# Performance work log

Measured on AMD Instinct MI355X. Metric: run time of the kernel, lower is better.

The kernel has to match this reference:

```python
import jax, jax.numpy as jnp
import numpy as np

N = 100000   # nodes
D = 128      # feature dim
E = 1600000  # edges (avg degree 16)
BN_EPS = 1e-5


def setup_inputs() -> dict:
    key = jax.random.key(0)
    ks = jax.random.split(key, 8)
    x = jax.random.normal(ks[0], (N, D), dtype=jnp.float32)
    edge_index = jax.random.randint(ks[1], (2, E), 0, N, dtype=jnp.int64)
    W = jax.random.normal(ks[2], (D, D), dtype=jnp.float32) * 0.05   # GCNConv linear weight
    b = jax.random.normal(ks[3], (D,), dtype=jnp.float32) * 0.05     # GCNConv bias
    gamma = jax.random.uniform(ks[4], (D,), dtype=jnp.float32) + 0.5 # BN weight
    beta = jax.random.normal(ks[5], (D,), dtype=jnp.float32) * 0.1   # BN bias
    running_mean = jax.random.normal(ks[6], (D,), dtype=jnp.float32) * 0.1
    running_var = jax.random.uniform(ks[7], (D,), dtype=jnp.float32) + 0.5
    return {"x": x, "edge_index": edge_index, "W": W, "b": b,
            "gamma": gamma, "beta": beta,
            "running_mean": running_mean, "running_var": running_var}


def reference(x, edge_index, W, b, gamma, beta, running_mean, running_var):
    # --- GCNConv (default: add self-loops, symmetric normalization) ---
    h = x @ W                                        # [N, D]
    loops = jnp.arange(N, dtype=edge_index.dtype)
    src = jnp.concatenate([edge_index[0], loops])    # [E+N]
    dst = jnp.concatenate([edge_index[1], loops])    # [E+N]
    deg = jax.ops.segment_sum(jnp.ones_like(dst, dtype=h.dtype), dst, num_segments=N)
    dinv = jax.lax.rsqrt(jnp.maximum(deg, 1.0))      # deg >= 1 due to self-loops
    norm = dinv[src] * dinv[dst]                     # [E+N]
    agg = jax.ops.segment_sum(h[src] * norm[:, None], dst, num_segments=N)  # [N, D]
    agg = agg + b
    # --- BatchNorm1d (inference: running stats) ---
    bn = (agg - running_mean) * jax.lax.rsqrt(running_var + BN_EPS) * gamma + beta
    # --- ReLU + residual (dropout is identity in eval) ---
    return jax.nn.relu(bn) + x
```

## Files before the change

kernel.cpp:

```cpp
#include <hip/hip_runtime.h>

#define D 128
#define BN_EPS 1e-5f
#define NBUCK 512
#define BSHIFT 8
#define BNODES 256

using short8 = __attribute__((ext_vector_type(8))) short;
using floatx4 = __attribute__((ext_vector_type(4))) float;

__device__ inline unsigned short f2bf(float f) {
    unsigned u = __float_as_uint(f);
    u += 0x7fff + ((u >> 16) & 1);
    return (unsigned short)(u >> 16);
}
__device__ inline float bf2f(unsigned short s) {
    return __uint_as_float(((unsigned)s) << 16);
}

__global__ void wt_kernel(const float* __restrict__ W, const float* __restrict__ b,
                          const float* __restrict__ gamma, const float* __restrict__ beta,
                          const float* __restrict__ mean, const float* __restrict__ var,
                          unsigned short* __restrict__ Wt, float* __restrict__ scv,
                          float* __restrict__ pov) {
    int t = blockIdx.x * blockDim.x + threadIdx.x;
    int k = t >> 7, n = t & 127;
    Wt[(size_t)n * D + k] = f2bf(W[t]);
    if (t < D) {
        float sc = gamma[t] * rsqrtf(var[t] + BN_EPS);
        scv[t] = sc;
        pov[t] = (b[t] - mean[t]) * sc + beta[t];
    }
}

__global__ __launch_bounds__(512) void pAwt_kernel(
    const int* __restrict__ dst, int* __restrict__ bucketTot, int E,
    const float* __restrict__ W, const float* __restrict__ b,
    const float* __restrict__ gamma, const float* __restrict__ beta,
    const float* __restrict__ mean, const float* __restrict__ var,
    unsigned short* __restrict__ Wt, float* __restrict__ scv,
    float* __restrict__ pov) {
    __shared__ int lh[NBUCK];
    int tid = threadIdx.x;
    lh[tid] = 0;
    __syncthreads();
    for (int i = blockIdx.x * 512 + tid; i < E; i += gridDim.x * 512)
        atomicAdd(&lh[dst[i] >> BSHIFT], 1);
    if (blockIdx.x < 16) {
        int t = blockIdx.x * 512 + tid;
#pragma unroll
        for (int h = 0; h < 2; ++h) {
            int tt = t + h * 8192;
            Wt[(size_t)(tt & 127) * D + (tt >> 7)] = f2bf(W[tt]);
        }
        if (blockIdx.x == 0 && tid < D) {
            float sc = gamma[tid] * rsqrtf(var[tid] + BN_EPS);
            scv[tid] = sc;
            pov[tid] = (b[tid] - mean[tid]) * sc + beta[tid];
        }
    }
    __syncthreads();
    if (lh[tid]) atomicAdd(&bucketTot[tid], lh[tid]);
}

__global__ __launch_bounds__(512) void pB_kernel(const int* __restrict__ src,
                                                 const int* __restrict__ dst,
                                                 const int* __restrict__ bucketTot,
                                                 int* __restrict__ resCnt,
                                                 int2* __restrict__ pairs, int E) {
    __shared__ int sb[NBUCK];
    __shared__ int lh[NBUCK];
    __shared__ int lcur[NBUCK];
    int tid = threadIdx.x;
    sb[tid] = bucketTot[tid];
    lh[tid] = 0;
    __syncthreads();
    for (int d = 1; d < NBUCK; d <<= 1) {
        int v = (tid >= d) ? sb[tid - d] : 0;
        __syncthreads();
        sb[tid] += v;
        __syncthreads();
    }
    int chunk = (E + gridDim.x - 1) / gridDim.x;
    int base = blockIdx.x * chunk;
    int lim = min(chunk, E - base);
    if (lim <= 0) return;
    for (int i = tid; i < lim; i += 512) atomicAdd(&lh[dst[base + i] >> BSHIFT], 1);
    __syncthreads();
    int c = lh[tid];
    lcur[tid] = c ? (sb[tid] - bucketTot[tid]) + atomicAdd(&resCnt[tid], c) : 0;
    __syncthreads();
    for (int i = tid; i < lim; i += 512) {
        int s = src[base + i], d2 = dst[base + i];
        int pos = atomicAdd(&lcur[d2 >> BSHIFT], 1);
        pairs[pos] = make_int2(s, d2);
    }
}

__global__ __launch_bounds__(512) void sortxs_kernel(
    const int2* __restrict__ pairs, const int* __restrict__ bucketTot,
    const float* __restrict__ x, int* __restrict__ deg, int* __restrict__ offs,
    int* __restrict__ colidx, float* __restrict__ dinv,
    unsigned short* __restrict__ xs, int N, int E) {
    __shared__ int sb[NBUCK];
    __shared__ int lh[BNODES];
    __shared__ int lcur[BNODES];
    __shared__ float sdv[BNODES];
    int tid = threadIdx.x;
    int b = blockIdx.x;
    sb[tid] = bucketTot[tid];
    __syncthreads();
    for (int d = 1; d < NBUCK; d <<= 1) {
        int v = (tid >= d) ? sb[tid - d] : 0;
        __syncthreads();
        sb[tid] += v;
        __syncthreads();
    }
    int cnt = bucketTot[b];
    int base = sb[b] - cnt;
    if (tid < BNODES) lh[tid] = 0;
    __syncthreads();
    for (int i = tid; i < cnt; i += 512)
        atomicAdd(&lh[pairs[base + i].y & (BNODES - 1)], 1);
    __syncthreads();
    int orig = (tid < BNODES) ? lh[tid] : 0;
    for (int d = 1; d < BNODES; d <<= 1) {
        int v = (tid < BNODES && tid >= d) ? lh[tid - d] : 0;
        __syncthreads();
        if (tid < BNODES) lh[tid] += v;
        __syncthreads();
    }
    if (tid < BNODES) {
        int exc = lh[tid] - orig;
        int node = b * BNODES + tid;
        float dvv = rsqrtf((float)(orig + 1));
        sdv[tid] = dvv;
        if (node < N) {
            deg[node] = orig;
            offs[node] = base + exc;
            dinv[node] = dvv;
        }
        lcur[tid] = exc;
    }
    if (b == 0 && tid == 0) offs[N] = E;
    __syncthreads();
    for (int i = tid; i < cnt; i += 512) {
        int2 p = pairs[base + i];
        int pos = atomicAdd(&lcur[p.y & (BNODES - 1)], 1);
        colidx[base + pos] = p.x;
    }
    int nb = min(BNODES, N - b * BNODES);
    if (nb > 0) {
        const float4* x4 = (const float4*)x;
        ushort4* xs4 = (ushort4*)xs;
        int tot = nb * 32;
        for (int c = tid; c < tot; c += 512) {
            int nl = c >> 5, q = c & 31;
            int node = b * BNODES + nl;
            float dvv = sdv[nl];
            float4 f = x4[(size_t)node * 32 + q];
            ushort4 o;
            o.x = f2bf(dvv * f.x); o.y = f2bf(dvv * f.y);
            o.z = f2bf(dvv * f.z); o.w = f2bf(dvv * f.w);
            xs4[(size_t)node * 32 + q] = o;
        }
    }
}

__global__ void deg_kernel(const int* __restrict__ dst, int* __restrict__ deg, int E) {
    int e = blockIdx.x * blockDim.x + threadIdx.x;
    if (e < E) atomicAdd(&deg[dst[e]], 1);
}

__global__ void dinv_kernel(const int* __restrict__ deg, float* __restrict__ dinv, int N) {
    int v = blockIdx.x * blockDim.x + threadIdx.x;
    if (v < N) dinv[v] = rsqrtf((float)(deg[v] + 1));
}

__global__ __launch_bounds__(256) void scan1_kernel(const int* __restrict__ deg,
                                                    int* __restrict__ bsum, int N) {
    __shared__ int s[256];
    int t = threadIdx.x;
    int v = blockIdx.x * 256 + t;
    s[t] = (v < N) ? deg[v] : 0;
    for (int st = 128; st > 0; st >>= 1) {
        __syncthreads();
        if (t < st) s[t] += s[t + st];
    }
    if (t == 0) bsum[blockIdx.x] = s[0];
}

__global__ __launch_bounds__(512) void scan2_kernel(int* __restrict__ bsum,
                                                    int* __restrict__ offs, int P, int N) {
    __shared__ int a[512];
    int t = threadIdx.x;
    int orig = (t < P) ? bsum[t] : 0;
    a[t] = orig;
    __syncthreads();
    for (int d = 1; d < 512; d <<= 1) {
        int tv = (t >= d) ? a[t - d] : 0;
        __syncthreads();
        a[t] += tv;
        __syncthreads();
    }
    if (t < P) bsum[t] = a[t] - orig;
    if (t == 0) offs[N] = a[511];
}

__global__ __launch_bounds__(256) void scan3_kernel(const int* __restrict__ deg,
                                                    const int* __restrict__ bsum,
                                                    int* __restrict__ offs,
                                                    int* __restrict__ cursor, int N) {
    __shared__ int a[256];
    int t = threadIdx.x;
    int v = blockIdx.x * 256 + t;
    int d = (v < N) ? deg[v] : 0;
    a[t] = d;
    __syncthreads();
    for (int st = 1; st < 256; st <<= 1) {
        int tv = (t >= st) ? a[t - st] : 0;
        __syncthreads();
        a[t] += tv;
        __syncthreads();
    }
    if (v < N) {
        int off = bsum[blockIdx.x] + a[t] - d;
        offs[v] = off;
        cursor[v] = off;
    }
}

__global__ void fill_kernel(const int* __restrict__ src, const int* __restrict__ dst,
                            int* __restrict__ cursor, int* __restrict__ colidx, int E) {
    int e = blockIdx.x * blockDim.x + threadIdx.x;
    if (e < E) {
        int d = dst[e];
        int pos = atomicAdd(&cursor[d], 1);
        colidx[pos] = src[e];
    }
}

__global__ __launch_bounds__(256) void agg_kernel(
    const float* __restrict__ x, const unsigned short* __restrict__ xs,
    const float* __restrict__ dinv, const int* __restrict__ offs,
    const int* __restrict__ colidx, float* __restrict__ outp,
    unsigned int* __restrict__ aggb, int N) {
    int wid = (blockIdx.x * blockDim.x + threadIdx.x) >> 6;
    if (wid >= N) return;
    int lane = threadIdx.x & 63;
    float dv = dinv[wid];
    float a0, a1;
    int p = offs[wid], pe = offs[wid + 1];
    if (xs) {
        const unsigned int* xs32 = (const unsigned int*)xs;
        unsigned int sv = xs32[(size_t)wid * 64 + lane];
        a0 = bf2f((unsigned short)sv);
        a1 = bf2f((unsigned short)(sv >> 16));
        for (; p + 16 <= pe; p += 16) {
            int u[16];
            unsigned int v[16];
#pragma unroll
            for (int j = 0; j < 16; ++j) u[j] = colidx[p + j];
#pragma unroll
            for (int j = 0; j < 16; ++j) v[j] = xs32[(size_t)u[j] * 64 + lane];
#pragma unroll
            for (int j = 0; j < 16; ++j) {
                a0 += bf2f((unsigned short)v[j]);
                a1 += bf2f((unsigned short)(v[j] >> 16));
            }
        }
        for (; p + 4 <= pe; p += 4) {
            int u[4];
            unsigned int v[4];
#pragma unroll
            for (int j = 0; j < 4; ++j) u[j] = colidx[p + j];
#pragma unroll
            for (int j = 0; j < 4; ++j) v[j] = xs32[(size_t)u[j] * 64 + lane];
#pragma unroll
            for (int j = 0; j < 4; ++j) {
                a0 += bf2f((unsigned short)v[j]);
                a1 += bf2f((unsigned short)(v[j] >> 16));
            }
        }
        for (; p < pe; ++p) {
            unsigned int v = xs32[(size_t)colidx[p] * 64 + lane];
            a0 += bf2f((unsigned short)v);
            a1 += bf2f((unsigned short)(v >> 16));
        }
        aggb[(size_t)wid * 64 + lane] =
            (unsigned int)f2bf(dv * a0) | ((unsigned int)f2bf(dv * a1) << 16);
    } else {
        const float2* x2 = (const float2*)x;
        float2 s = x2[(size_t)wid * 64 + lane];
        a0 = dv * s.x;
        a1 = dv * s.y;
        for (; p < pe; ++p) {
            int u = colidx[p];
            float du = dinv[u];
            float2 vv = x2[(size_t)u * 64 + lane];
            a0 += du * vv.x;
            a1 += du * vv.y;
        }
        float2 r;
        r.x = dv * a0;
        r.y = dv * a1;
        ((float2*)outp)[(size_t)wid * 64 + lane] = r;
    }
}

__global__ __launch_bounds__(256) void gemm_kernel(
    float* __restrict__ outp, const float* __restrict__ xg,
    const unsigned short* __restrict__ Wt, const unsigned short* __restrict__ aggb,
    const float* __restrict__ scv, const float* __restrict__ pov, int nTiles) {
    __shared__ uint4 sW4[2048];
    int tid = threadIdx.x;
    const uint4* W4 = (const uint4*)Wt;
#pragma unroll
    for (int i = 0; i < 8; ++i) {
        int q = tid + i * 256;
        int row = q >> 4, c4 = q & 15;
        sW4[row * 16 + (c4 ^ (row & 7))] = W4[q];
    }
    __syncthreads();

    int wid = (blockIdx.x * blockDim.x + tid) >> 6;
    if (wid >= nTiles) return;
    int lane = tid & 63;
    int m = lane & 15, quad = lane >> 4;
    int row0 = wid * 16;

    short8 A[4];
    if (aggb) {
        const unsigned short* arow = aggb + (size_t)(row0 + m) * D;
#pragma unroll
        for (int ks = 0; ks < 4; ++ks)
            A[ks] = *(const short8*)&arow[ks * 32 + quad * 8];
    } else {
        const float* arow = outp + (size_t)(row0 + m) * D;
#pragma unroll
        for (int ks = 0; ks < 4; ++ks) {
            float4 f0 = *(const float4*)(arow + ks * 32 + quad * 8);
            float4 f1 = *(const float4*)(arow + ks * 32 + quad * 8 + 4);
            short8 af;
            af[0] = (short)f2bf(f0.x); af[1] = (short)f2bf(f0.y);
            af[2] = (short)f2bf(f0.z); af[3] = (short)f2bf(f0.w);
            af[4] = (short)f2bf(f1.x); af[5] = (short)f2bf(f1.y);
            af[6] = (short)f2bf(f1.z); af[7] = (short)f2bf(f1.w);
            A[ks] = af;
        }
    }

#pragma unroll
    for (int cg = 0; cg < 8; ++cg) {
        int brow = cg * 16 + m;
        floatx4 acc = {0.f, 0.f, 0.f, 0.f};
#pragma unroll
        for (int ks = 0; ks < 4; ++ks) {
            short8 Bf = *(const short8*)&sW4[brow * 16 + ((ks * 4 + quad) ^ (m & 7))];
            acc = __builtin_amdgcn_mfma_f32_16x16x32_bf16(A[ks], Bf, acc, 0, 0, 0);
        }
        int col = cg * 16 + m;
        float sc = scv[col], po = pov[col];
#pragma unroll
        for (int i = 0; i < 4; ++i) {
            int row = row0 + quad * 4 + i;
            float bn = acc[i] * sc + po;
            size_t idx = (size_t)row * D + col;
            outp[idx] = fmaxf(bn, 0.f) + xg[idx];
        }
    }
}

extern "C" void kernel_launch(void* const* d_in, const int* in_sizes, int n_in,
                              void* d_out, int out_size, void* d_ws, size_t ws_size,
                              hipStream_t stream) {
    const float* x = (const float*)d_in[0];
    const int* edge = (const int*)d_in[1];
    const float* Wm = (const float*)d_in[2];
    const float* b = (const float*)d_in[3];
    const float* gamma = (const float*)d_in[4];
    const float* beta = (const float*)d_in[5];
    const float* mean = (const float*)d_in[6];
    const float* var = (const float*)d_in[7];
    float* out = (float*)d_out;

    int N = in_sizes[0] / D;
    int E = in_sizes[1] / 2;
    const int* src = edge;
    const int* dst = edge + E;
    int P = (N + 255) / 256;

    char* w = (char*)d_ws;
    size_t cur = 0;
    auto take = [&](size_t bytes) -> void* {
        cur = (cur + 15) & ~(size_t)15;
        void* p = w + cur;
        cur += bytes;
        return p;
    };
    int* deg = (int*)take((size_t)N * 4);
    int* bucketTot = (int*)take(NBUCK * 4);
    int* resCnt = (int*)take(NBUCK * 4);
    float* dinv = (float*)take((size_t)N * 4);
    int* offs = (int*)take((size_t)(N + 1) * 4);
    int* cursor = (int*)take((size_t)N * 4);
    int* bsum = (int*)take((size_t)(P + 1) * 4);
    unsigned short* Wt = (unsigned short*)take((size_t)D * D * 2);
    float* scv = (float*)take(D * 4);
    float* pov = (float*)take(D * 4);
    int* colidx = (int*)take((size_t)E * 4);
    cur = (cur + 15) & ~(size_t)15;
    size_t fixedEnd = cur;

    size_t xsBytes = (size_t)N * D * 2;
    size_t zoneBytes = (xsBytes > (size_t)E * 8) ? xsBytes : (size_t)E * 8;
    bool fast = fixedEnd + xsBytes + zoneBytes <= ws_size;

    unsigned short* xs = nullptr;
    int2* pairs = nullptr;
    unsigned int* aggb = nullptr;
    if (fast) {
        xs = (unsigned short*)(w + fixedEnd);
        pairs = (int2*)(w + fixedEnd + xsBytes);
        aggb = (unsigned int*)(w + fixedEnd + xsBytes);
    }

    if (fast) {
        hipMemsetAsync(bucketTot, 0, (size_t)NBUCK * 8, stream);
        pAwt_kernel<<<1024, 512, 0, stream>>>(dst, bucketTot, E, Wm, b, gamma, beta,
                                              mean, var, Wt, scv, pov);
        pB_kernel<<<1024, 512, 0, stream>>>(src, dst, bucketTot, resCnt, pairs, E);
        sortxs_kernel<<<NBUCK, 512, 0, stream>>>(pairs, bucketTot, x, deg, offs, colidx,
                                                 dinv, xs, N, E);
    } else {
        wt_kernel<<<(D * D) / 256, 256, 0, stream>>>(Wm, b, gamma, beta, mean, var, Wt,
                                                     scv, pov);
        hipMemsetAsync(deg, 0, sizeof(int) * N, stream);
        deg_kernel<<<(E + 255) / 256, 256, 0, stream>>>(dst, deg, E);
        dinv_kernel<<<(N + 255) / 256, 256, 0, stream>>>(deg, dinv, N);
        scan1_kernel<<<P, 256, 0, stream>>>(deg, bsum, N);
        scan2_kernel<<<1, 512, 0, stream>>>(bsum, offs, P, N);
        scan3_kernel<<<P, 256, 0, stream>>>(deg, bsum, offs, cursor, N);
        fill_kernel<<<(E + 255) / 256, 256, 0, stream>>>(src, dst, cursor, colidx, E);
    }
    agg_kernel<<<(N * 64 + 255) / 256, 256, 0, stream>>>(x, xs, dinv, offs, colidx, out,
                                                         aggb, N);
    int nTiles = (N + 15) / 16;
    gemm_kernel<<<(nTiles * 64 + 255) / 256, 256, 0, stream>>>(
        out, x, Wt, (const unsigned short*)aggb, scv, pov, nTiles);
}
```

Measured before the change: 286.7 us.

## Fuse aggregation with MFMA GEMM epilogue and move bf16 x conversion earlier

Aggregation and the GEMM are merged into one kernel. Each block aggregates 16 nodes into shared memory as bf16, then runs MFMA against Wt and applies the BN/ReLU/residual epilogue, so the intermediate aggregate no longer makes a round trip through global memory. The bf16 conversion of x moves into the first histogram kernel and no longer folds in dinv. The gather loop now loads per-neighbour dinv and uses a masked 16-wide tail. This costs an extra dinv gather per edge and fewer waves per node, since each wave handles 4 nodes serially.

```diff
diff --git a/kernel.cpp b/kernel.cpp
--- a/kernel.cpp
+++ b/kernel.cpp
@@ -39,13 +39,23 @@
     const float* __restrict__ gamma, const float* __restrict__ beta,
     const float* __restrict__ mean, const float* __restrict__ var,
     unsigned short* __restrict__ Wt, float* __restrict__ scv,
-    float* __restrict__ pov) {
+    float* __restrict__ pov, const float* __restrict__ x,
+    unsigned short* __restrict__ xs, int total4) {
     __shared__ int lh[NBUCK];
     int tid = threadIdx.x;
     lh[tid] = 0;
     __syncthreads();
     for (int i = blockIdx.x * 512 + tid; i < E; i += gridDim.x * 512)
         atomicAdd(&lh[dst[i] >> BSHIFT], 1);
+    const float4* x4 = (const float4*)x;
+    ushort4* xs4 = (ushort4*)xs;
+    for (int i = blockIdx.x * 512 + tid; i < total4; i += gridDim.x * 512) {
+        float4 f = x4[i];
+        ushort4 o;
+        o.x = f2bf(f.x); o.y = f2bf(f.y);
+        o.z = f2bf(f.z); o.w = f2bf(f.w);
+        xs4[i] = o;
+    }
     if (blockIdx.x < 16) {
         int t = blockIdx.x * 512 + tid;
 #pragma unroll
@@ -97,15 +107,13 @@
     }
 }
 
-__global__ __launch_bounds__(512) void sortxs_kernel(
+__global__ __launch_bounds__(512) void sort_kernel(
     const int2* __restrict__ pairs, const int* __restrict__ bucketTot,
-    const float* __restrict__ x, int* __restrict__ deg, int* __restrict__ offs,
-    int* __restrict__ colidx, float* __restrict__ dinv,
-    unsigned short* __restrict__ xs, int N, int E) {
+    int* __restrict__ offs, int* __restrict__ colidx, float* __restrict__ dinv,
+    int N, int E) {
     __shared__ int sb[NBUCK];
     __shared__ int lh[BNODES];
     __shared__ int lcur[BNODES];
-    __shared__ float sdv[BNODES];
     int tid = threadIdx.x;
     int b = blockIdx.x;
     sb[tid] = bucketTot[tid];
@@ -133,12 +141,9 @@
     if (tid < BNODES) {
         int exc = lh[tid] - orig;
         int node = b * BNODES + tid;
-        float dvv = rsqrtf((float)(orig + 1));
-        sdv[tid] = dvv;
         if (node < N) {
-            deg[node] = orig;
             offs[node] = base + exc;
-            dinv[node] = dvv;
+            dinv[node] = rsqrtf((float)(orig + 1));
         }
         lcur[tid] = exc;
     }
@@ -148,22 +153,6 @@
         int2 p = pairs[base + i];
         int pos = atomicAdd(&lcur[p.y & (BNODES - 1)], 1);
         colidx[base + pos] = p.x;
-    }
-    int nb = min(BNODES, N - b * BNODES);
-    if (nb > 0) {
-        const float4* x4 = (const float4*)x;
-        ushort4* xs4 = (ushort4*)xs;
-        int tot = nb * 32;
-        for (int c = tid; c < tot; c += 512) {
-            int nl = c >> 5, q = c & 31;
-            int node = b * BNODES + nl;
-            float dvv = sdv[nl];
-            float4 f = x4[(size_t)node * 32 + q];
-            ushort4 o;
-            o.x = f2bf(dvv * f.x); o.y = f2bf(dvv * f.y);
-            o.z = f2bf(dvv * f.z); o.w = f2bf(dvv * f.w);
-            xs4[(size_t)node * 32 + q] = o;
-        }
     }
 }
 
@@ -241,77 +230,35 @@
 }
 
 __global__ __launch_bounds__(256) void agg_kernel(
-    const float* __restrict__ x, const unsigned short* __restrict__ xs,
-    const float* __restrict__ dinv, const int* __restrict__ offs,
-    const int* __restrict__ colidx, float* __restrict__ outp,
-    unsigned int* __restrict__ aggb, int N) {
+    const float* __restrict__ x, const float* __restrict__ dinv,
+    const int* __restrict__ offs, const int* __restrict__ colidx,
+    float* __restrict__ outp, int N) {
     int wid = (blockIdx.x * blockDim.x + threadIdx.x) >> 6;
     if (wid >= N) return;
     int lane = threadIdx.x & 63;
     float dv = dinv[wid];
-    float a0, a1;
     int p = offs[wid], pe = offs[wid + 1];
-    if (xs) {
-        const unsigned int* xs32 = (const unsigned int*)xs;
-        unsigned int sv = xs32[(size_t)wid * 64 + lane];
-        a0 = bf2f((unsigned short)sv);
-        a1 = bf2f((unsigned short)(sv >> 16));
-        for (; p + 16 <= pe; p += 16) {
-            int u[16];
-            unsigned int v[16];
-#pragma unroll
-            for (int j = 0; j < 16; ++j) u[j] = colidx[p + j];
-#pragma unroll
-            for (int j = 0; j < 16; ++j) v[j] = xs32[(size_t)u[j] * 64 + lane];
-#pragma unroll
-            for (int j = 0; j < 16; ++j) {
-                a0 += bf2f((unsigned short)v[j]);
-                a1 += bf2f((unsigned short)(v[j] >> 16));
-            }
-        }
-        for (; p + 4 <= pe; p += 4) {
-            int u[4];
-            unsigned int v[4];
-#pragma unroll
-            for (int j = 0; j < 4; ++j) u[j] = colidx[p + j];
-#pragma unroll
-            for (int j = 0; j < 4; ++j) v[j] = xs32[(size_t)u[j] * 64 + lane];
-#pragma unroll
-            for (int j = 0; j < 4; ++j) {
-                a0 += bf2f((unsigned short)v[j]);
-                a1 += bf2f((unsigned short)(v[j] >> 16));
-            }
-        }
-        for (; p < pe; ++p) {
-            unsigned int v = xs32[(size_t)colidx[p] * 64 + lane];
-            a0 += bf2f((unsigned short)v);
-            a1 += bf2f((unsigned short)(v >> 16));
-        }
-        aggb[(size_t)wid * 64 + lane] =
-            (unsigned int)f2bf(dv * a0) | ((unsigned int)f2bf(dv * a1) << 16);
-    } else {
-        const float2* x2 = (const float2*)x;
-        float2 s = x2[(size_t)wid * 64 + lane];
-        a0 = dv * s.x;
-        a1 = dv * s.y;
-        for (; p < pe; ++p) {
-            int u = colidx[p];
-            float du = dinv[u];
-            float2 vv = x2[(size_t)u * 64 + lane];
-            a0 += du * vv.x;
-            a1 += du * vv.y;
-        }
-        float2 r;
-        r.x = dv * a0;
-        r.y = dv * a1;
-        ((float2*)outp)[(size_t)wid * 64 + lane] = r;
-    }
+    const float2* x2 = (const float2*)x;
+    float2 s = x2[(size_t)wid * 64 + lane];
+    float a0 = dv * s.x;
+    float a1 = dv * s.y;
+    for (; p < pe; ++p) {
+        int u = colidx[p];
+        float du = dinv[u];
+        float2 vv = x2[(size_t)u * 64 + lane];
+        a0 += du * vv.x;
+        a1 += du * vv.y;
+    }
+    float2 r;
+    r.x = dv * a0;
+    r.y = dv * a1;
+    ((float2*)outp)[(size_t)wid * 64 + lane] = r;
 }
 
 __global__ __launch_bounds__(256) void gemm_kernel(
     float* __restrict__ outp, const float* __restrict__ xg,
-    const unsigned short* __restrict__ Wt, const unsigned short* __restrict__ aggb,
-    const float* __restrict__ scv, const float* __restrict__ pov, int nTiles) {
+    const unsigned short* __restrict__ Wt, const float* __restrict__ scv,
+    const float* __restrict__ pov, int nTiles) {
     __shared__ uint4 sW4[2048];
     int tid = threadIdx.x;
     const uint4* W4 = (const uint4*)Wt;
@@ -330,24 +277,17 @@
     int row0 = wid * 16;
 
     short8 A[4];
-    if (aggb) {
-        const unsigned short* arow = aggb + (size_t)(row0 + m) * D;
-#pragma unroll
-        for (int ks = 0; ks < 4; ++ks)
-            A[ks] = *(const short8*)&arow[ks * 32 + quad * 8];
-    } else {
-        const float* arow = outp + (size_t)(row0 + m) * D;
-#pragma unroll
-        for (int ks = 0; ks < 4; ++ks) {
-            float4 f0 = *(const float4*)(arow + ks * 32 + quad * 8);
-            float4 f1 = *(const float4*)(arow + ks * 32 + quad * 8 + 4);
-            short8 af;
-            af[0] = (short)f2bf(f0.x); af[1] = (short)f2bf(f0.y);
-            af[2] = (short)f2bf(f0.z); af[3] = (short)f2bf(f0.w);
-            af[4] = (short)f2bf(f1.x); af[5] = (short)f2bf(f1.y);
-            af[6] = (short)f2bf(f1.z); af[7] = (short)f2bf(f1.w);
-            A[ks] = af;
-        }
+    const float* arow = outp + (size_t)(row0 + m) * D;
+#pragma unroll
+    for (int ks = 0; ks < 4; ++ks) {
+        float4 f0 = *(const float4*)(arow + ks * 32 + quad * 8);
+        float4 f1 = *(const float4*)(arow + ks * 32 + quad * 8 + 4);
+        short8 af;
+        af[0] = (short)f2bf(f0.x); af[1] = (short)f2bf(f0.y);
+        af[2] = (short)f2bf(f0.z); af[3] = (short)f2bf(f0.w);
+        af[4] = (short)f2bf(f1.x); af[5] = (short)f2bf(f1.y);
+        af[6] = (short)f2bf(f1.z); af[7] = (short)f2bf(f1.w);
+        A[ks] = af;
     }
 
 #pragma unroll
@@ -367,6 +307,106 @@
             float bn = acc[i] * sc + po;
             size_t idx = (size_t)row * D + col;
             outp[idx] = fmaxf(bn, 0.f) + xg[idx];
+        }
+    }
+}
+
+__global__ __launch_bounds__(256) void aggemm_kernel(
+    const unsigned short* __restrict__ xs, const float* __restrict__ dinv,
+    const int* __restrict__ offs, const int* __restrict__ colidx,
+    const float* __restrict__ xg, const unsigned short* __restrict__ Wt,
+    const float* __restrict__ scv, const float* __restrict__ pov,
+    float* __restrict__ outp, int N) {
+    __shared__ unsigned int sA[16][68];
+    int tid = threadIdx.x;
+    int lane = tid & 63;
+    int w = tid >> 6;
+    int row0 = blockIdx.x * 16;
+    const unsigned int* xs32 = (const unsigned int*)xs;
+
+#pragma unroll
+    for (int k = 0; k < 4; ++k) {
+        int nl = w * 4 + k;
+        int node = row0 + nl;
+        if (node < N) {
+            float dv = dinv[node];
+            unsigned int sv = xs32[(size_t)node * 64 + lane];
+            float a0 = dv * bf2f((unsigned short)sv);
+            float a1 = dv * bf2f((unsigned short)(sv >> 16));
+            int p = offs[node], pe = offs[node + 1];
+            for (; p + 16 <= pe; p += 16) {
+                int u[16];
+                float du[16];
+                unsigned int v[16];
+#pragma unroll
+                for (int j = 0; j < 16; ++j) u[j] = colidx[p + j];
+#pragma unroll
+                for (int j = 0; j < 16; ++j) du[j] = dinv[u[j]];
+#pragma unroll
+                for (int j = 0; j < 16; ++j) v[j] = xs32[(size_t)u[j] * 64 + lane];
+#pragma unroll
+                for (int j = 0; j < 16; ++j) {
+                    a0 = fmaf(du[j], bf2f((unsigned short)v[j]), a0);
+                    a1 = fmaf(du[j], bf2f((unsigned short)(v[j] >> 16)), a1);
+                }
+            }
+            int rem = pe - p;
+            if (rem > 0) {
+                int u[16];
+                float du[16];
+                unsigned int v[16];
+#pragma unroll
+                for (int j = 0; j < 16; ++j) u[j] = (j < rem) ? colidx[p + j] : 0;
+#pragma unroll
+                for (int j = 0; j < 16; ++j) du[j] = (j < rem) ? dinv[u[j]] : 0.f;
+#pragma unroll
+                for (int j = 0; j < 16; ++j)
+                    v[j] = (j < rem) ? xs32[(size_t)u[j] * 64 + lane] : 0u;
+#pragma unroll
+                for (int j = 0; j < 16; ++j) {
+                    a0 = fmaf(du[j], bf2f((unsigned short)v[j]), a0);
+                    a1 = fmaf(du[j], bf2f((unsigned short)(v[j] >> 16)), a1);
+                }
+            }
+            sA[nl][lane] = (unsigned int)f2bf(dv * a0) |
+                           ((unsigned int)f2bf(dv * a1) << 16);
+        } else {
+            sA[nl][lane] = 0u;
+        }
+    }
+    __syncthreads();
+
+    int m = lane & 15, quad = lane >> 4;
+    short8 B[2][4];
+#pragma unroll
+    for (int c = 0; c < 2; ++c) {
+        int brow = (w * 2 + c) * 16 + m;
+#pragma unroll
+        for (int ks = 0; ks < 4; ++ks)
+            B[c][ks] = *(const short8*)&Wt[(size_t)brow * D + ks * 32 + quad * 8];
+    }
+    short8 A[4];
+#pragma unroll
+    for (int ks = 0; ks < 4; ++ks)
+        A[ks] = *(const short8*)&sA[m][ks * 16 + quad * 4];
+
+#pragma unroll
+    for (int c = 0; c < 2; ++c) {
+        floatx4 acc = {0.f, 0.f, 0.f, 0.f};
+#pragma unroll
+        for (int ks = 0; ks < 4; ++ks)
+            acc = __builtin_amdgcn_mfma_f32_16x16x32_bf16(A[ks], B[c][ks], acc, 0, 0, 0);
+        int col = (w * 2 + c) * 16 + m;
+        float sc = scv[col], po = pov[col];
+#pragma unroll
+        for (int i = 0; i < 4; ++i) {
+            int row = row0 + quad * 4 + i;
+            if (row < N) {
+                float bn = acc[i] * sc + po;
+                size_t idx = (size_t)row * D + col;
+                float xr = __builtin_nontemporal_load(xg + idx);
+                __builtin_nontemporal_store(fmaxf(bn, 0.f) + xr, outp + idx);
+            }
         }
     }
 }
@@ -418,20 +458,20 @@
 
     unsigned short* xs = nullptr;
     int2* pairs = nullptr;
-    unsigned int* aggb = nullptr;
     if (fast) {
         xs = (unsigned short*)(w + fixedEnd);
         pairs = (int2*)(w + fixedEnd + xsBytes);
-        aggb = (unsigned int*)(w + fixedEnd + xsBytes);
     }
 
     if (fast) {
         hipMemsetAsync(bucketTot, 0, (size_t)NBUCK * 8, stream);
         pAwt_kernel<<<1024, 512, 0, stream>>>(dst, bucketTot, E, Wm, b, gamma, beta,
-                                              mean, var, Wt, scv, pov);
+                                              mean, var, Wt, scv, pov, x, xs, N * 32);
         pB_kernel<<<1024, 512, 0, stream>>>(src, dst, bucketTot, resCnt, pairs, E);
-        sortxs_kernel<<<NBUCK, 512, 0, stream>>>(pairs, bucketTot, x, deg, offs, colidx,
-                                                 dinv, xs, N, E);
+        sort_kernel<<<NBUCK, 512, 0, stream>>>(pairs, bucketTot, offs, colidx, dinv, N,
+                                               E);
+        aggemm_kernel<<<(N + 15) / 16, 256, 0, stream>>>(xs, dinv, offs, colidx, x, Wt,
+                                                         scv, pov, out, N);
     } else {
         wt_kernel<<<(D * D) / 256, 256, 0, stream>>>(Wm, b, gamma, beta, mean, var, Wt,
                                                      scv, pov);
@@ -442,10 +482,10 @@
         scan2_kernel<<<1, 512, 0, stream>>>(bsum, offs, P, N);
         scan3_kernel<<<P, 256, 0, stream>>>(deg, bsum, offs, cursor, N);
         fill_kernel<<<(E + 255) / 256, 256, 0, stream>>>(src, dst, cursor, colidx, E);
-    }
-    agg_kernel<<<(N * 64 + 255) / 256, 256, 0, stream>>>(x, xs, dinv, offs, colidx, out,
-                                                         aggb, N);
-    int nTiles = (N + 15) / 16;
-    gemm_kernel<<<(nTiles * 64 + 255) / 256, 256, 0, stream>>>(
-        out, x, Wt, (const unsigned short*)aggb, scv, pov, nTiles);
-}
+        agg_kernel<<<(N * 64 + 255) / 256, 256, 0, stream>>>(x, dinv, offs, colidx, out,
+                                                             N);
+        int nTiles = (N + 15) / 16;
+        gemm_kernel<<<(nTiles * 64 + 255) / 256, 256, 0, stream>>>(out, x, Wt, scv, pov,
+                                                                   nTiles);
+    }
+}
```

After: 348.0 us. +21.4%, slower.

## Fuse preprocessing into one cooperative kernel and apply source norm in aggregation

Applied to the files above, without the earlier changes.

Replaces the memset plus three preprocessing kernels (bucket histogram, bucket scatter, per-bucket sort) with a single cooperative kernel of 512 blocks that uses grid-wide syncs between phases. This removes launch gaps and lets the x-to-bf16 conversion run alongside the histogram instead of after the sort. Because dinv is no longer known when xs is written, xs now holds unscaled bf16 x, and the aggregation kernel gathers dinv[u] per neighbor and applies it with an fma. The cost is an extra random dinv load per edge, and only 512 resident blocks run the edge-heavy phases.

```diff
diff --git a/kernel.cpp b/kernel.cpp
--- a/kernel.cpp
+++ b/kernel.cpp
@@ -1,4 +1,7 @@
 #include <hip/hip_runtime.h>
+#include <hip/hip_cooperative_groups.h>
+
+namespace cg = cooperative_groups;
 
 #define D 128
 #define BN_EPS 1e-5f
@@ -16,6 +19,123 @@
 }
 __device__ inline float bf2f(unsigned short s) {
     return __uint_as_float(((unsigned)s) << 16);
+}
+
+__global__ __launch_bounds__(512, 4) void prep_kernel(
+    const int* __restrict__ src, const int* __restrict__ dst, int E, int N,
+    const float* __restrict__ W, const float* __restrict__ b,
+    const float* __restrict__ gamma, const float* __restrict__ beta,
+    const float* __restrict__ mean, const float* __restrict__ var,
+    unsigned short* __restrict__ Wt, float* __restrict__ scv,
+    float* __restrict__ pov, const float* __restrict__ x,
+    unsigned short* __restrict__ xs, int total4,
+    int* __restrict__ bucketTot, int* __restrict__ resCnt,
+    int2* __restrict__ pairs, int* __restrict__ offs,
+    int* __restrict__ colidx, float* __restrict__ dinv) {
+    cg::grid_group grid = cg::this_grid();
+    __shared__ int sb[NBUCK];
+    __shared__ int lh[NBUCK];
+    __shared__ int lcur[NBUCK];
+    int tid = threadIdx.x;
+    int bid = blockIdx.x;
+    int gsz = gridDim.x;
+    int gt = bid * 512 + tid;
+
+    if (gt < NBUCK) {
+        bucketTot[gt] = 0;
+        resCnt[gt] = 0;
+    }
+    grid.sync();
+
+    lh[tid] = 0;
+    __syncthreads();
+    for (int i = gt; i < E; i += gsz * 512)
+        atomicAdd(&lh[dst[i] >> BSHIFT], 1);
+    {
+        const float4* x4 = (const float4*)x;
+        ushort4* xs4 = (ushort4*)xs;
+        for (int i = gt; i < total4; i += gsz * 512) {
+            float4 f = x4[i];
+            ushort4 o;
+            o.x = f2bf(f.x); o.y = f2bf(f.y);
+            o.z = f2bf(f.z); o.w = f2bf(f.w);
+            xs4[i] = o;
+        }
+    }
+    if (bid < 16) {
+        int t = bid * 512 + tid;
+#pragma unroll
+        for (int h = 0; h < 2; ++h) {
+            int tt = t + h * 8192;
+            Wt[(size_t)(tt & 127) * D + (tt >> 7)] = f2bf(W[tt]);
+        }
+        if (bid == 0 && tid < D) {
+            float sc = gamma[tid] * rsqrtf(var[tid] + BN_EPS);
+            scv[tid] = sc;
+            pov[tid] = (b[tid] - mean[tid]) * sc + beta[tid];
+        }
+    }
+    __syncthreads();
+    if (lh[tid]) atomicAdd(&bucketTot[tid], lh[tid]);
+    grid.sync();
+
+    sb[tid] = bucketTot[tid];
+    lh[tid] = 0;
+    __syncthreads();
+    for (int d = 1; d < NBUCK; d <<= 1) {
+        int v = (tid >= d) ? sb[tid - d] : 0;
+        __syncthreads();
+        sb[tid] += v;
+        __syncthreads();
+    }
+    int chunk = (E + gsz - 1) / gsz;
+    int base = bid * chunk;
+    int lim = min(chunk, E - base);
+    if (lim > 0) {
+        for (int i = tid; i < lim; i += 512)
+            atomicAdd(&lh[dst[base + i] >> BSHIFT], 1);
+        __syncthreads();
+        int c = lh[tid];
+        lcur[tid] = c ? (sb[tid] - bucketTot[tid]) + atomicAdd(&resCnt[tid], c) : 0;
+        __syncthreads();
+        for (int i = tid; i < lim; i += 512) {
+            int s = src[base + i], d2 = dst[base + i];
+            int pos = atomicAdd(&lcur[d2 >> BSHIFT], 1);
+            pairs[pos] = make_int2(s, d2);
+        }
+    }
+    grid.sync();
+
+    int cnt = bucketTot[bid];
+    int bbase = sb[bid] - cnt;
+    if (tid < BNODES) lh[tid] = 0;
+    __syncthreads();
+    for (int i = tid; i < cnt; i += 512)
+        atomicAdd(&lh[pairs[bbase + i].y & (BNODES - 1)], 1);
+    __syncthreads();
+    int orig = (tid < BNODES) ? lh[tid] : 0;
+    for (int d = 1; d < BNODES; d <<= 1) {
+        int v = (tid < BNODES && tid >= d) ? lh[tid - d] : 0;
+        __syncthreads();
+        if (tid < BNODES) lh[tid] += v;
+        __syncthreads();
+    }
+    if (tid < BNODES) {
+        int exc = lh[tid] - orig;
+        int node = bid * BNODES + tid;
+        if (node < N) {
+            offs[node] = bbase + exc;
+            dinv[node] = rsqrtf((float)(orig + 1));
+        }
+        lcur[tid] = exc;
+    }
+    if (bid == 0 && tid == 0) offs[N] = E;
+    __syncthreads();
+    for (int i = tid; i < cnt; i += 512) {
+        int2 p = pairs[bbase + i];
+        int pos = atomicAdd(&lcur[p.y & (BNODES - 1)], 1);
+        colidx[bbase + pos] = p.x;
+    }
 }
 
 __global__ void wt_kernel(const float* __restrict__ W, const float* __restrict__ b,
@@ -30,140 +150,6 @@
         float sc = gamma[t] * rsqrtf(var[t] + BN_EPS);
         scv[t] = sc;
         pov[t] = (b[t] - mean[t]) * sc + beta[t];
-    }
-}
-
-__global__ __launch_bounds__(512) void pAwt_kernel(
-    const int* __restrict__ dst, int* __restrict__ bucketTot, int E,
-    const float* __restrict__ W, const float* __restrict__ b,
-    const float* __restrict__ gamma, const float* __restrict__ beta,
-    const float* __restrict__ mean, const float* __restrict__ var,
-    unsigned short* __restrict__ Wt, float* __restrict__ scv,
-    float* __restrict__ pov) {
-    __shared__ int lh[NBUCK];
-    int tid = threadIdx.x;
-    lh[tid] = 0;
-    __syncthreads();
-    for (int i = blockIdx.x * 512 + tid; i < E; i += gridDim.x * 512)
-        atomicAdd(&lh[dst[i] >> BSHIFT], 1);
-    if (blockIdx.x < 16) {
-        int t = blockIdx.x * 512 + tid;
-#pragma unroll
-        for (int h = 0; h < 2; ++h) {
-            int tt = t + h * 8192;
-            Wt[(size_t)(tt & 127) * D + (tt >> 7)] = f2bf(W[tt]);
-        }
-        if (blockIdx.x == 0 && tid < D) {
-            float sc = gamma[tid] * rsqrtf(var[tid] + BN_EPS);
-            scv[tid] = sc;
-            pov[tid] = (b[tid] - mean[tid]) * sc + beta[tid];
-        }
-    }
-    __syncthreads();
-    if (lh[tid]) atomicAdd(&bucketTot[tid], lh[tid]);
-}
-
-__global__ __launch_bounds__(512) void pB_kernel(const int* __restrict__ src,
-                                                 const int* __restrict__ dst,
-                                                 const int* __restrict__ bucketTot,
-                                                 int* __restrict__ resCnt,
-                                                 int2* __restrict__ pairs, int E) {
-    __shared__ int sb[NBUCK];
-    __shared__ int lh[NBUCK];
-    __shared__ int lcur[NBUCK];
-    int tid = threadIdx.x;
-    sb[tid] = bucketTot[tid];
-    lh[tid] = 0;
-    __syncthreads();
-    for (int d = 1; d < NBUCK; d <<= 1) {
-        int v = (tid >= d) ? sb[tid - d] : 0;
-        __syncthreads();
-        sb[tid] += v;
-        __syncthreads();
-    }
-    int chunk = (E + gridDim.x - 1) / gridDim.x;
-    int base = blockIdx.x * chunk;
-    int lim = min(chunk, E - base);
-    if (lim <= 0) return;
-    for (int i = tid; i < lim; i += 512) atomicAdd(&lh[dst[base + i] >> BSHIFT], 1);
-    __syncthreads();
-    int c = lh[tid];
-    lcur[tid] = c ? (sb[tid] - bucketTot[tid]) + atomicAdd(&resCnt[tid], c) : 0;
-    __syncthreads();
-    for (int i = tid; i < lim; i += 512) {
-        int s = src[base + i], d2 = dst[base + i];
-        int pos = atomicAdd(&lcur[d2 >> BSHIFT], 1);
-        pairs[pos] = make_int2(s, d2);
-    }
-}
-
-__global__ __launch_bounds__(512) void sortxs_kernel(
-    const int2* __restrict__ pairs, const int* __restrict__ bucketTot,
-    const float* __restrict__ x, int* __restrict__ deg, int* __restrict__ offs,
-    int* __restrict__ colidx, float* __restrict__ dinv,
-    unsigned short* __restrict__ xs, int N, int E) {
-    __shared__ int sb[NBUCK];
-    __shared__ int lh[BNODES];
-    __shared__ int lcur[BNODES];
-    __shared__ float sdv[BNODES];
-    int tid = threadIdx.x;
-    int b = blockIdx.x;
-    sb[tid] = bucketTot[tid];
-    __syncthreads();
-    for (int d = 1; d < NBUCK; d <<= 1) {
-        int v = (tid >= d) ? sb[tid - d] : 0;
-        __syncthreads();
-        sb[tid] += v;
-        __syncthreads();
-    }
-    int cnt = bucketTot[b];
-    int base = sb[b] - cnt;
-    if (tid < BNODES) lh[tid] = 0;
-    __syncthreads();
-    for (int i = tid; i < cnt; i += 512)
-        atomicAdd(&lh[pairs[base + i].y & (BNODES - 1)], 1);
-    __syncthreads();
-    int orig = (tid < BNODES) ? lh[tid] : 0;
-    for (int d = 1; d < BNODES; d <<= 1) {
-        int v = (tid < BNODES && tid >= d) ? lh[tid - d] : 0;
-        __syncthreads();
-        if (tid < BNODES) lh[tid] += v;
-        __syncthreads();
-    }
-    if (tid < BNODES) {
-        int exc = lh[tid] - orig;
-        int node = b * BNODES + tid;
-        float dvv = rsqrtf((float)(orig + 1));
-        sdv[tid] = dvv;
-        if (node < N) {
-            deg[node] = orig;
-            offs[node] = base + exc;
-            dinv[node] = dvv;
-        }
-        lcur[tid] = exc;
-    }
-    if (b == 0 && tid == 0) offs[N] = E;
-    __syncthreads();
-    for (int i = tid; i < cnt; i += 512) {
-        int2 p = pairs[base + i];
-        int pos = atomicAdd(&lcur[p.y & (BNODES - 1)], 1);
-        colidx[base + pos] = p.x;
-    }
-    int nb = min(BNODES, N - b * BNODES);
-    if (nb > 0) {
-        const float4* x4 = (const float4*)x;
-        ushort4* xs4 = (ushort4*)xs;
-        int tot = nb * 32;
-        for (int c = tid; c < tot; c += 512) {
-            int nl = c >> 5, q = c & 31;
-            int node = b * BNODES + nl;
-            float dvv = sdv[nl];
-            float4 f = x4[(size_t)node * 32 + q];
-            ushort4 o;
-            o.x = f2bf(dvv * f.x); o.y = f2bf(dvv * f.y);
-            o.z = f2bf(dvv * f.z); o.w = f2bf(dvv * f.w);
-            xs4[(size_t)node * 32 + q] = o;
-        }
     }
 }
 
@@ -254,38 +240,46 @@
     if (xs) {
         const unsigned int* xs32 = (const unsigned int*)xs;
         unsigned int sv = xs32[(size_t)wid * 64 + lane];
-        a0 = bf2f((unsigned short)sv);
-        a1 = bf2f((unsigned short)(sv >> 16));
+        a0 = dv * bf2f((unsigned short)sv);
+        a1 = dv * bf2f((unsigned short)(sv >> 16));
         for (; p + 16 <= pe; p += 16) {
             int u[16];
+            float du[16];
             unsigned int v[16];
 #pragma unroll
             for (int j = 0; j < 16; ++j) u[j] = colidx[p + j];
 #pragma unroll
             for (int j = 0; j < 16; ++j) v[j] = xs32[(size_t)u[j] * 64 + lane];
 #pragma unroll
+            for (int j = 0; j < 16; ++j) du[j] = dinv[u[j]];
+#pragma unroll
             for (int j = 0; j < 16; ++j) {
-                a0 += bf2f((unsigned short)v[j]);
-                a1 += bf2f((unsigned short)(v[j] >> 16));
+                a0 = fmaf(du[j], bf2f((unsigned short)v[j]), a0);
+                a1 = fmaf(du[j], bf2f((unsigned short)(v[j] >> 16)), a1);
             }
         }
         for (; p + 4 <= pe; p += 4) {
             int u[4];
+            float du[4];
             unsigned int v[4];
 #pragma unroll
             for (int j = 0; j < 4; ++j) u[j] = colidx[p + j];
 #pragma unroll
             for (int j = 0; j < 4; ++j) v[j] = xs32[(size_t)u[j] * 64 + lane];
 #pragma unroll
+            for (int j = 0; j < 4; ++j) du[j] = dinv[u[j]];
+#pragma unroll
             for (int j = 0; j < 4; ++j) {
-                a0 += bf2f((unsigned short)v[j]);
-                a1 += bf2f((unsigned short)(v[j] >> 16));
+                a0 = fmaf(du[j], bf2f((unsigned short)v[j]), a0);
+                a1 = fmaf(du[j], bf2f((unsigned short)(v[j] >> 16)), a1);
             }
         }
         for (; p < pe; ++p) {
-            unsigned int v = xs32[(size_t)colidx[p] * 64 + lane];
-            a0 += bf2f((unsigned short)v);
-            a1 += bf2f((unsigned short)(v >> 16));
+            int u = colidx[p];
+            float du = dinv[u];
+            unsigned int v = xs32[(size_t)u * 64 + lane];
+            a0 = fmaf(du, bf2f((unsigned short)v), a0);
+            a1 = fmaf(du, bf2f((unsigned short)(v >> 16)), a1);
         }
         aggb[(size_t)wid * 64 + lane] =
             (unsigned int)f2bf(dv * a0) | ((unsigned int)f2bf(dv * a1) << 16);
@@ -351,15 +345,15 @@
     }
 
 #pragma unroll
-    for (int cg = 0; cg < 8; ++cg) {
-        int brow = cg * 16 + m;
+    for (int cg2 = 0; cg2 < 8; ++cg2) {
+        int brow = cg2 * 16 + m;
         floatx4 acc = {0.f, 0.f, 0.f, 0.f};
 #pragma unroll
         for (int ks = 0; ks < 4; ++ks) {
             short8 Bf = *(const short8*)&sW4[brow * 16 + ((ks * 4 + quad) ^ (m & 7))];
             acc = __builtin_amdgcn_mfma_f32_16x16x32_bf16(A[ks], Bf, acc, 0, 0, 0);
         }
-        int col = cg * 16 + m;
+        int col = cg2 * 16 + m;
         float sc = scv[col], po = pov[col];
 #pragma unroll
         for (int i = 0; i < 4; ++i) {
@@ -426,12 +420,21 @@
     }
 
     if (fast) {
-        hipMemsetAsync(bucketTot, 0, (size_t)NBUCK * 8, stream);
-        pAwt_kernel<<<1024, 512, 0, stream>>>(dst, bucketTot, E, Wm, b, gamma, beta,
-                                              mean, var, Wt, scv, pov);
-        pB_kernel<<<1024, 512, 0, stream>>>(src, dst, bucketTot, resCnt, pairs, E);
-        sortxs_kernel<<<NBUCK, 512, 0, stream>>>(pairs, bucketTot, x, deg, offs, colidx,
-                                                 dinv, xs, N, E);
+        int total4 = N * 32;
+        void* args[] = {
+            (void*)&src, (void*)&dst, (void*)&E, (void*)&N,
+            (void*)&Wm, (void*)&b, (void*)&gamma, (void*)&beta,
+            (void*)&mean, (void*)&var, (void*)&Wt, (void*)&scv,
+            (void*)&pov, (void*)&x, (void*)&xs, (void*)&total4,
+            (void*)&bucketTot, (void*)&resCnt, (void*)&pairs,
+            (void*)&offs, (void*)&colidx, (void*)&dinv};
+        hipLaunchCooperativeKernel((const void*)prep_kernel, dim3(NBUCK), dim3(512),
+                                   args, 0, stream);
+        agg_kernel<<<(N * 64 + 255) / 256, 256, 0, stream>>>(x, xs, dinv, offs, colidx,
+                                                             out, aggb, N);
+        int nTiles = (N + 15) / 16;
+        gemm_kernel<<<(nTiles * 64 + 255) / 256, 256, 0, stream>>>(
+            out, x, Wt, (const unsigned short*)aggb, scv, pov, nTiles);
     } else {
         wt_kernel<<<(D * D) / 256, 256, 0, stream>>>(Wm, b, gamma, beta, mean, var, Wt,
                                                      scv, pov);
@@ -442,10 +445,10 @@
         scan2_kernel<<<1, 512, 0, stream>>>(bsum, offs, P, N);
         scan3_kernel<<<P, 256, 0, stream>>>(deg, bsum, offs, cursor, N);
         fill_kernel<<<(E + 255) / 256, 256, 0, stream>>>(src, dst, cursor, colidx, E);
-    }
-    agg_kernel<<<(N * 64 + 255) / 256, 256, 0, stream>>>(x, xs, dinv, offs, colidx, out,
-                                                         aggb, N);
-    int nTiles = (N + 15) / 16;
-    gemm_kernel<<<(nTiles * 64 + 255) / 256, 256, 0, stream>>>(
-        out, x, Wt, (const unsigned short*)aggb, scv, pov, nTiles);
-}
+        agg_kernel<<<(N * 64 + 255) / 256, 256, 0, stream>>>(x, nullptr, dinv, offs,
+                                                             colidx, out, nullptr, N);
+        int nTiles = (N + 15) / 16;
+        gemm_kernel<<<(nTiles * 64 + 255) / 256, 256, 0, stream>>>(out, x, Wt, nullptr,
+                                                                   scv, pov, nTiles);
+    }
+}
```

Result: slower. 468.1 us (+63.3%).
